# Kernel optimization log

Measured on AMD Instinct MI355X. Metric: run time of the kernel, lower is better.

The kernel has to match this reference:

```python
import jax, jax.numpy as jnp
import numpy as np

N = 16384
E = 65536

def _nnconv(x, src, dst, edge_attr, A, b, root, bias, c_in, c_out):
    # edge MLP: [E,2] -> [E, c_in*c_out], ReLU
    W = jax.nn.relu(edge_attr @ A + b).reshape(E, c_in, c_out)
    # gather source features, per-edge matmul: [E,c_in] x [E,c_in,c_out] -> [E,c_out]
    msg = jnp.einsum('ei,eio->eo', x[src], W)
    # scatter-add to target nodes
    agg = jax.ops.segment_sum(msg, dst, num_segments=N)
    return agg + x @ root + bias

def setup_inputs() -> dict:
    key = jax.random.key(0)
    ks = jax.random.split(key, 12)
    inp = {
        'x': jax.random.normal(ks[0], (N, 8), dtype=jnp.float32),
        'edge_index': jax.random.randint(ks[1], (2, E), 0, N, dtype=jnp.int64),
        'edge_attr': jax.random.normal(ks[2], (E, 2), dtype=jnp.float32),
        # edge-MLP 1: Linear(2, 512)
        'A1': jax.random.normal(ks[3], (2, 512), dtype=jnp.float32) * (1.0 / np.sqrt(2.0)),
        'b1': jnp.zeros((512,), dtype=jnp.float32),
        # edge-MLP 2: Linear(2, 4096)
        'A2': jax.random.normal(ks[4], (2, 4096), dtype=jnp.float32) * (1.0 / np.sqrt(2.0)),
        'b2': jnp.zeros((4096,), dtype=jnp.float32),
        # NNConv root weights + biases
        'root1': jax.random.normal(ks[5], (8, 64), dtype=jnp.float32) * (1.0 / np.sqrt(8.0)),
        'bias1': jnp.zeros((64,), dtype=jnp.float32),
        'root2': jax.random.normal(ks[6], (64, 64), dtype=jnp.float32) * (1.0 / np.sqrt(64.0)),
        'bias2': jnp.zeros((64,), dtype=jnp.float32),
    }
    return inp

def reference(x, edge_index, edge_attr, A1, b1, A2, b2, root1, bias1, root2, bias2):
    src = edge_index[0]  # x_j (message source)
    dst = edge_index[1]  # aggregation target
    h = _nnconv(x, src, dst, edge_attr, A1, b1, root1, bias1, 8, 64)
    h = _nnconv(h, src, dst, edge_attr, A2, b2, root2, bias2, 64, 64)
    return h
```

## Files before the change

### kernel.cpp

```cpp
#include <hip/hip_runtime.h>

#define N_NODES 16384
#define N_EDGES 65536

typedef float f32x16 __attribute__((ext_vector_type(16)));
typedef float f32x8  __attribute__((ext_vector_type(8)));

__device__ __forceinline__ float rfl_f(float v) {
    int i = __builtin_amdgcn_readfirstlane(__builtin_bit_cast(int, v));
    return __builtin_bit_cast(float, i);
}

__global__ void k_node1(const float* __restrict__ x, const float* __restrict__ root1,
                        const float* __restrict__ bias1, float* __restrict__ h1) {
    int t = blockIdx.x * blockDim.x + threadIdx.x;
    int n = t >> 6, o = t & 63;
    float acc = bias1[o];
#pragma unroll
    for (int i = 0; i < 8; ++i)
        acc = fmaf(x[n * 8 + i], root1[i * 64 + o], acc);
    h1[t] = acc;
}

__global__ __launch_bounds__(256)
void k_edge1(const float* __restrict__ x, const int* __restrict__ ei,
             const float* __restrict__ ea, const float* __restrict__ A1,
             const float* __restrict__ b1, float* __restrict__ h1) {
    int lane = threadIdx.x & 63;
    float w0[8], w1[8], bb[8];
#pragma unroll
    for (int i = 0; i < 8; ++i) {
        w0[i] = A1[i * 64 + lane];
        w1[i] = A1[512 + i * 64 + lane];
        bb[i] = b1[i * 64 + lane];
    }
#pragma unroll
    for (int i = 0; i < 8; ++i)
        asm volatile("" : "+v"(w0[i]), "+v"(w1[i]), "+v"(bb[i]));

    int wid = blockIdx.x * (blockDim.x >> 6) + (threadIdx.x >> 6);
    int nw = gridDim.x * (blockDim.x >> 6);
    for (int e = wid; e < N_EDGES; e += nw) {
        int src = __builtin_amdgcn_readfirstlane(ei[e]);
        int dst = __builtin_amdgcn_readfirstlane(ei[N_EDGES + e]);
        float2 eav = ((const float2*)ea)[e];
        float ea0 = rfl_f(eav.x), ea1 = rfl_f(eav.y);
        const float* xp = x + (size_t)src * 8;
        f32x8 h;
        asm volatile("s_load_dwordx8 %0, %1, 0x0\n\t"
                     "s_waitcnt lgkmcnt(0)"
                     : "=s"(h) : "s"(xp));
        float acc = 0.f;
#pragma unroll
        for (int i = 0; i < 8; ++i) {
            float wv = fmaxf(fmaf(ea1, w1[i], fmaf(ea0, w0[i], bb[i])), 0.f);
            acc = fmaf(h[i], wv, acc);
        }
        atomicAdd(&h1[(size_t)dst * 64 + lane], acc);
    }
}

__global__ __launch_bounds__(256)
void k_node2(const float* __restrict__ h1, const float* __restrict__ root2,
             const float* __restrict__ bias2, float* __restrict__ out) {
    int lane = threadIdx.x & 63;
    float r[64];
#pragma unroll
    for (int i = 0; i < 64; ++i) r[i] = root2[i * 64 + lane];
#pragma unroll
    for (int i = 0; i < 64; ++i) asm volatile("" : "+v"(r[i]));
    float bias = bias2[lane];

    int wid = blockIdx.x * (blockDim.x >> 6) + (threadIdx.x >> 6);
    int nw = gridDim.x * (blockDim.x >> 6);
    for (int n = wid; n < N_NODES; n += nw) {
        int nu = __builtin_amdgcn_readfirstlane(n);
        const float* hp = h1 + (size_t)nu * 64;
        f32x16 h0, h1v, h2, h3;
        asm volatile("s_load_dwordx16 %0, %4, 0x0\n\t"
                     "s_load_dwordx16 %1, %4, 0x40\n\t"
                     "s_load_dwordx16 %2, %4, 0x80\n\t"
                     "s_load_dwordx16 %3, %4, 0xc0\n\t"
                     "s_waitcnt lgkmcnt(0)"
                     : "=s"(h0), "=s"(h1v), "=s"(h2), "=s"(h3) : "s"(hp));
        float acc = bias;
#pragma unroll
        for (int i = 0; i < 16; ++i) acc = fmaf(h0[i],  r[i],      acc);
#pragma unroll
        for (int i = 0; i < 16; ++i) acc = fmaf(h1v[i], r[16 + i], acc);
#pragma unroll
        for (int i = 0; i < 16; ++i) acc = fmaf(h2[i],  r[32 + i], acc);
#pragma unroll
        for (int i = 0; i < 16; ++i) acc = fmaf(h3[i],  r[48 + i], acc);
        out[(size_t)nu * 64 + lane] = acc;
    }
}

__global__ __launch_bounds__(64, 2)
void k_edge2(const float* __restrict__ h1, const int* __restrict__ ei,
             const float* __restrict__ ea, const float* __restrict__ A2,
             const float* __restrict__ b2, float* __restrict__ out) {
    int lane = threadIdx.x;
    float w0[64], w1[64], bb[64];
#pragma unroll
    for (int i = 0; i < 64; ++i) {
        w0[i] = A2[i * 64 + lane];
        w1[i] = A2[4096 + i * 64 + lane];
        bb[i] = b2[i * 64 + lane];
    }
#pragma unroll
    for (int i = 0; i < 64; ++i)
        asm volatile("" : "+v"(w0[i]), "+v"(w1[i]), "+v"(bb[i]));

#pragma clang loop unroll(disable)
    for (int e = blockIdx.x; e < N_EDGES; e += gridDim.x) {
        int src = __builtin_amdgcn_readfirstlane(ei[e]);
        int dst = __builtin_amdgcn_readfirstlane(ei[N_EDGES + e]);
        float2 eav = ((const float2*)ea)[e];
        float ea0 = rfl_f(eav.x), ea1 = rfl_f(eav.y);
        const float* hp = h1 + (size_t)src * 64;
        f32x16 h0, h1v, h2, h3;
        asm volatile("s_load_dwordx16 %0, %4, 0x0\n\t"
                     "s_load_dwordx16 %1, %4, 0x40\n\t"
                     "s_load_dwordx16 %2, %4, 0x80\n\t"
                     "s_load_dwordx16 %3, %4, 0xc0\n\t"
                     "s_waitcnt lgkmcnt(0)"
                     : "=s"(h0), "=s"(h1v), "=s"(h2), "=s"(h3) : "s"(hp));
        float acc = 0.f;
#pragma unroll
        for (int i = 0; i < 16; ++i) {
            float wv = fmaxf(fmaf(ea1, w1[i], fmaf(ea0, w0[i], bb[i])), 0.f);
            acc = fmaf(h0[i], wv, acc);
        }
#pragma unroll
        for (int i = 0; i < 16; ++i) {
            float wv = fmaxf(fmaf(ea1, w1[16 + i], fmaf(ea0, w0[16 + i], bb[16 + i])), 0.f);
            acc = fmaf(h1v[i], wv, acc);
        }
#pragma unroll
        for (int i = 0; i < 16; ++i) {
            float wv = fmaxf(fmaf(ea1, w1[32 + i], fmaf(ea0, w0[32 + i], bb[32 + i])), 0.f);
            acc = fmaf(h2[i], wv, acc);
        }
#pragma unroll
        for (int i = 0; i < 16; ++i) {
            float wv = fmaxf(fmaf(ea1, w1[48 + i], fmaf(ea0, w0[48 + i], bb[48 + i])), 0.f);
            acc = fmaf(h3[i], wv, acc);
        }
        atomicAdd(&out[(size_t)dst * 64 + lane], acc);
    }
}

extern "C" void kernel_launch(void* const* d_in, const int* in_sizes, int n_in,
                              void* d_out, int out_size, void* d_ws, size_t ws_size,
                              hipStream_t stream) {
    const float* x     = (const float*)d_in[0];
    const int*   ei    = (const int*)d_in[1];
    const float* ea    = (const float*)d_in[2];
    const float* A1    = (const float*)d_in[3];
    const float* b1    = (const float*)d_in[4];
    const float* A2    = (const float*)d_in[5];
    const float* b2    = (const float*)d_in[6];
    const float* root1 = (const float*)d_in[7];
    const float* bias1 = (const float*)d_in[8];
    const float* root2 = (const float*)d_in[9];
    const float* bias2 = (const float*)d_in[10];
    float* out = (float*)d_out;
    float* h1  = (float*)d_ws;

    k_node1<<<N_NODES * 64 / 256, 256, 0, stream>>>(x, root1, bias1, h1);
    k_edge1<<<2048, 256, 0, stream>>>(x, ei, ea, A1, b1, h1);
    k_node2<<<1024, 256, 0, stream>>>(h1, root2, bias2, out);
    k_edge2<<<2048, 64, 0, stream>>>(h1, ei, ea, A2, b2, out);
}
```

Measured before the change: 147.5 us.

## Split edge2 input channels across wave pairs and process two edges per wave

In the second edge kernel, each pair of waves now splits the 64 input channels in half. Each wave keeps only 32 rows of the edge-MLP weights in registers, which cuts VGPR pressure and allows 256-thread blocks with higher occupancy. Both edge kernels now handle two edges per iteration, using vector loads for indices and attributes and issuing two scalar gathers together to hide latency. The cost is twice as many atomic adds in edge2, since each wave-half contributes a partial sum per edge.

```diff
diff --git a/kernel.cpp b/kernel.cpp
--- a/kernel.cpp
+++ b/kernel.cpp
@@ -40,23 +40,34 @@
 
     int wid = blockIdx.x * (blockDim.x >> 6) + (threadIdx.x >> 6);
     int nw = gridDim.x * (blockDim.x >> 6);
-    for (int e = wid; e < N_EDGES; e += nw) {
-        int src = __builtin_amdgcn_readfirstlane(ei[e]);
-        int dst = __builtin_amdgcn_readfirstlane(ei[N_EDGES + e]);
-        float2 eav = ((const float2*)ea)[e];
-        float ea0 = rfl_f(eav.x), ea1 = rfl_f(eav.y);
-        const float* xp = x + (size_t)src * 8;
-        f32x8 h;
-        asm volatile("s_load_dwordx8 %0, %1, 0x0\n\t"
+#pragma clang loop unroll(disable)
+    for (int p = wid; p < N_EDGES / 2; p += nw) {
+        int2 srcp = ((const int2*)ei)[p];
+        int2 dstp = ((const int2*)(ei + N_EDGES))[p];
+        float4 eap = ((const float4*)ea)[p];
+        int s0 = __builtin_amdgcn_readfirstlane(srcp.x);
+        int s1 = __builtin_amdgcn_readfirstlane(srcp.y);
+        int d0 = __builtin_amdgcn_readfirstlane(dstp.x);
+        int d1 = __builtin_amdgcn_readfirstlane(dstp.y);
+        float ea00 = rfl_f(eap.x), ea01 = rfl_f(eap.y);
+        float ea10 = rfl_f(eap.z), ea11 = rfl_f(eap.w);
+        const float* xp0 = x + (size_t)s0 * 8;
+        const float* xp1 = x + (size_t)s1 * 8;
+        f32x8 ha, hb;
+        asm volatile("s_load_dwordx8 %0, %2, 0x0\n\t"
+                     "s_load_dwordx8 %1, %3, 0x0\n\t"
                      "s_waitcnt lgkmcnt(0)"
-                     : "=s"(h) : "s"(xp));
-        float acc = 0.f;
+                     : "=s"(ha), "=s"(hb) : "s"(xp0), "s"(xp1));
+        float acc0 = 0.f, acc1 = 0.f;
 #pragma unroll
         for (int i = 0; i < 8; ++i) {
-            float wv = fmaxf(fmaf(ea1, w1[i], fmaf(ea0, w0[i], bb[i])), 0.f);
-            acc = fmaf(h[i], wv, acc);
+            float wva = fmaxf(fmaf(ea01, w1[i], fmaf(ea00, w0[i], bb[i])), 0.f);
+            acc0 = fmaf(ha[i], wva, acc0);
+            float wvb = fmaxf(fmaf(ea11, w1[i], fmaf(ea10, w0[i], bb[i])), 0.f);
+            acc1 = fmaf(hb[i], wvb, acc1);
         }
-        atomicAdd(&h1[(size_t)dst * 64 + lane], acc);
+        atomicAdd(&h1[(size_t)d0 * 64 + lane], acc0);
+        atomicAdd(&h1[(size_t)d1 * 64 + lane], acc1);
     }
 }
 
@@ -96,58 +107,65 @@
     }
 }
 
-__global__ __launch_bounds__(64, 2)
+__global__ __launch_bounds__(256)
 void k_edge2(const float* __restrict__ h1, const int* __restrict__ ei,
              const float* __restrict__ ea, const float* __restrict__ A2,
              const float* __restrict__ b2, float* __restrict__ out) {
-    int lane = threadIdx.x;
-    float w0[64], w1[64], bb[64];
+    int lane = threadIdx.x & 63;
+    int wid = blockIdx.x * (blockDim.x >> 6) + (threadIdx.x >> 6);
+    int nw = gridDim.x * (blockDim.x >> 6);
+    int base = __builtin_amdgcn_readfirstlane((wid & 1) * 32);
+
+    float w0[32], w1[32], bb[32];
 #pragma unroll
-    for (int i = 0; i < 64; ++i) {
-        w0[i] = A2[i * 64 + lane];
-        w1[i] = A2[4096 + i * 64 + lane];
-        bb[i] = b2[i * 64 + lane];
+    for (int i = 0; i < 32; ++i) {
+        int ii = base + i;
+        w0[i] = A2[ii * 64 + lane];
+        w1[i] = A2[4096 + ii * 64 + lane];
+        bb[i] = b2[ii * 64 + lane];
     }
 #pragma unroll
-    for (int i = 0; i < 64; ++i)
+    for (int i = 0; i < 32; ++i)
         asm volatile("" : "+v"(w0[i]), "+v"(w1[i]), "+v"(bb[i]));
 
 #pragma clang loop unroll(disable)
-    for (int e = blockIdx.x; e < N_EDGES; e += gridDim.x) {
-        int src = __builtin_amdgcn_readfirstlane(ei[e]);
-        int dst = __builtin_amdgcn_readfirstlane(ei[N_EDGES + e]);
-        float2 eav = ((const float2*)ea)[e];
-        float ea0 = rfl_f(eav.x), ea1 = rfl_f(eav.y);
-        const float* hp = h1 + (size_t)src * 64;
-        f32x16 h0, h1v, h2, h3;
+    for (int p = wid >> 1; p < N_EDGES / 2; p += (nw >> 1)) {
+        int2 srcp = ((const int2*)ei)[p];
+        int2 dstp = ((const int2*)(ei + N_EDGES))[p];
+        float4 eap = ((const float4*)ea)[p];
+        int s0 = __builtin_amdgcn_readfirstlane(srcp.x);
+        int s1 = __builtin_amdgcn_readfirstlane(srcp.y);
+        int d0 = __builtin_amdgcn_readfirstlane(dstp.x);
+        int d1 = __builtin_amdgcn_readfirstlane(dstp.y);
+        float ea00 = rfl_f(eap.x), ea01 = rfl_f(eap.y);
+        float ea10 = rfl_f(eap.z), ea11 = rfl_f(eap.w);
+        const float* hp0 = h1 + (size_t)s0 * 64 + base;
+        const float* hp1 = h1 + (size_t)s1 * 64 + base;
+        f32x16 ha, hb, hc, hd;
         asm volatile("s_load_dwordx16 %0, %4, 0x0\n\t"
                      "s_load_dwordx16 %1, %4, 0x40\n\t"
-                     "s_load_dwordx16 %2, %4, 0x80\n\t"
-                     "s_load_dwordx16 %3, %4, 0xc0\n\t"
+                     "s_load_dwordx16 %2, %5, 0x0\n\t"
+                     "s_load_dwordx16 %3, %5, 0x40\n\t"
                      "s_waitcnt lgkmcnt(0)"
-                     : "=s"(h0), "=s"(h1v), "=s"(h2), "=s"(h3) : "s"(hp));
-        float acc = 0.f;
+                     : "=s"(ha), "=s"(hb), "=s"(hc), "=s"(hd)
+                     : "s"(hp0), "s"(hp1));
+        float acc0 = 0.f, acc1 = 0.f;
 #pragma unroll
         for (int i = 0; i < 16; ++i) {
-            float wv = fmaxf(fmaf(ea1, w1[i], fmaf(ea0, w0[i], bb[i])), 0.f);
-            acc = fmaf(h0[i], wv, acc);
+            float wva = fmaxf(fmaf(ea01, w1[i], fmaf(ea00, w0[i], bb[i])), 0.f);
+            acc0 = fmaf(ha[i], wva, acc0);
+            float wvb = fmaxf(fmaf(ea11, w1[i], fmaf(ea10, w0[i], bb[i])), 0.f);
+            acc1 = fmaf(hc[i], wvb, acc1);
         }
 #pragma unroll
         for (int i = 0; i < 16; ++i) {
-            float wv = fmaxf(fmaf(ea1, w1[16 + i], fmaf(ea0, w0[16 + i], bb[16 + i])), 0.f);
-            acc = fmaf(h1v[i], wv, acc);
+            float wva = fmaxf(fmaf(ea01, w1[16 + i], fmaf(ea00, w0[16 + i], bb[16 + i])), 0.f);
+            acc0 = fmaf(hb[i], wva, acc0);
+            float wvb = fmaxf(fmaf(ea11, w1[16 + i], fmaf(ea10, w0[16 + i], bb[16 + i])), 0.f);
+            acc1 = fmaf(hd[i], wvb, acc1);
         }
-#pragma unroll
-        for (int i = 0; i < 16; ++i) {
-            float wv = fmaxf(fmaf(ea1, w1[32 + i], fmaf(ea0, w0[32 + i], bb[32 + i])), 0.f);
-            acc = fmaf(h2[i], wv, acc);
-        }
-#pragma unroll
-        for (int i = 0; i < 16; ++i) {
-            float wv = fmaxf(fmaf(ea1, w1[48 + i], fmaf(ea0, w0[48 + i], bb[48 + i])), 0.f);
-            acc = fmaf(h3[i], wv, acc);
-        }
-        atomicAdd(&out[(size_t)dst * 64 + lane], acc);
+        atomicAdd(&out[(size_t)d0 * 64 + lane], acc0);
+        atomicAdd(&out[(size_t)d1 * 64 + lane], acc1);
     }
 }
 
@@ -171,5 +189,5 @@
     k_node1<<<N_NODES * 64 / 256, 256, 0, stream>>>(x, root1, bias1, h1);
     k_edge1<<<2048, 256, 0, stream>>>(x, ei, ea, A1, b1, h1);
     k_node2<<<1024, 256, 0, stream>>>(h1, root2, bias2, out);
-    k_edge2<<<2048, 64, 0, stream>>>(h1, ei, ea, A2, b2, out);
+    k_edge2<<<2048, 256, 0, stream>>>(h1, ei, ea, A2, b2, out);
 }
```

After: 142.8 us. -3.2%, faster.
